# Optimization experiments

Measured on AMD Instinct MI355X. Metric: run time of the kernel, lower is better.

The kernel has to match this reference:

```python
import jax, jax.numpy as jnp
import numpy as np

B, I, K, O = 128, 64, 1024, 1024  # batch, kept in-axis, reduced in-axis, out-axis

def setup_inputs() -> dict:
    key = jax.random.key(0)
    k1, k2, k3 = jax.random.split(key, 3)
    stdv = 1.0 / np.sqrt(float(K))  # reduction covers in_shape[-1:] = [K]
    x = jax.random.normal(k1, (B, I, K), dtype=jnp.float32)
    weight = jax.random.uniform(k2, (O, I, K), dtype=jnp.float32, minval=-stdv, maxval=stdv)
    b = jax.random.uniform(k3, (O, I), dtype=jnp.float32, minval=-stdv, maxval=stdv)
    return {"x": x, "weight": weight, "b": b}

def reference(x, weight, b):
    # torch: unsqueeze x to [B,1,I,K], multiply by weight [O,I,K], sum last `reduction`=1
    # axes -> [B,O,I], add bias [O,I]. Expressed as a fused contraction:
    z = jnp.einsum('bik,oik->boi', x, weight)
    return z + b  # bias broadcasts over batch
```

## Files before the change

### kernel.cpp

```cpp
#include <hip/hip_runtime.h>

typedef __attribute__((ext_vector_type(8))) short  shortx8;
typedef __attribute__((ext_vector_type(4))) short  shortx4;
typedef __attribute__((ext_vector_type(4))) float  floatx4;

#define I_SZ 64
#define K_SZ 1024
#define IK   65536
#define OI   65536
#define BK   128
#define NKT  (K_SZ / BK)
#define LROW 256

__device__ __forceinline__ unsigned short f2bf(float f) {
    unsigned int u = __builtin_bit_cast(unsigned int, f);
    u += 0x7fffu + ((u >> 16) & 1u);
    return (unsigned short)(u >> 16);
}

__device__ __forceinline__ shortx4 cvt4(float4 a) {
    shortx4 r;
    r[0] = (short)f2bf(a.x); r[1] = (short)f2bf(a.y);
    r[2] = (short)f2bf(a.z); r[3] = (short)f2bf(a.w);
    return r;
}

__global__ __launch_bounds__(256, 2) void factlin_mfma2(
    const float* __restrict__ x, const float* __restrict__ w,
    const float* __restrict__ bias, float* __restrict__ out)
{
    __shared__ __align__(16) char lA[128 * LROW];
    __shared__ __align__(16) char lB[128 * LROW];

    const int wg   = blockIdx.x;
    const int nt   = wg & 7;
    const int i    = wg >> 3;
    const int tid  = threadIdx.x;
    const int lane = tid & 63;
    const int wid  = tid >> 6;
    const int wm   = wid >> 1;
    const int wn   = wid & 1;
    const int lrow = lane & 15;
    const int g    = lane >> 4;

    const float* gA = x + i * K_SZ;
    const float* gB = w + (nt * 128) * IK + i * K_SZ;

    floatx4 acc[4][4] = {};

    #pragma unroll 1
    for (int kt = 0; kt < NKT; ++kt) {
        __syncthreads();

        float4 buf[8];
        #pragma unroll
        for (int grp = 0; grp < 2; ++grp) {
            #pragma unroll
            for (int e = 0; e < 8; ++e) {
                const int c = (grp * 8 + e) * 256 + tid;
                buf[e] = *(const float4*)(gA + (c >> 5) * IK + kt * BK + (c & 31) * 4);
            }
            #pragma unroll
            for (int e = 0; e < 8; ++e) {
                const int c = (grp * 8 + e) * 256 + tid;
                const int row = c >> 5;
                const int off = row * LROW + (((c & 31) * 8) ^ ((row & 7) << 4));
                *(shortx4*)(lA + off) = cvt4(buf[e]);
            }
        }
        #pragma unroll
        for (int grp = 0; grp < 2; ++grp) {
            #pragma unroll
            for (int e = 0; e < 8; ++e) {
                const int c = (grp * 8 + e) * 256 + tid;
                buf[e] = *(const float4*)(gB + (c >> 5) * IK + kt * BK + (c & 31) * 4);
            }
            #pragma unroll
            for (int e = 0; e < 8; ++e) {
                const int c = (grp * 8 + e) * 256 + tid;
                const int row = c >> 5;
                const int off = row * LROW + (((c & 31) * 8) ^ ((row & 7) << 4));
                *(shortx4*)(lB + off) = cvt4(buf[e]);
            }
        }

        __syncthreads();

        #pragma unroll
        for (int ks = 0; ks < 4; ++ks) {
            shortx8 af[4], bf[4];
            #pragma unroll
            for (int mi = 0; mi < 4; ++mi) {
                const int row = wm * 64 + mi * 16 + lrow;
                const int off = row * LROW + ((ks * 64 + g * 16) ^ ((row & 7) << 4));
                af[mi] = *(const shortx8*)(lA + off);
            }
            #pragma unroll
            for (int ni = 0; ni < 4; ++ni) {
                const int row = wn * 64 + ni * 16 + lrow;
                const int off = row * LROW + ((ks * 64 + g * 16) ^ ((row & 7) << 4));
                bf[ni] = *(const shortx8*)(lB + off);
            }
            #pragma unroll
            for (int mi = 0; mi < 4; ++mi)
                #pragma unroll
                for (int ni = 0; ni < 4; ++ni)
                    acc[mi][ni] = __builtin_amdgcn_mfma_f32_16x16x32_bf16(
                        af[mi], bf[ni], acc[mi][ni], 0, 0, 0);
        }
    }

    const int obase = nt * 128 + wn * 64;
    float bv[4];
    #pragma unroll
    for (int ni = 0; ni < 4; ++ni)
        bv[ni] = bias[(obase + ni * 16 + lrow) * I_SZ + i];

    const int rb = wm * 64 + g * 4;
    #pragma unroll
    for (int mi = 0; mi < 4; ++mi) {
        #pragma unroll
        for (int ni = 0; ni < 4; ++ni) {
            const int ocol = obase + ni * 16 + lrow;
            float* op = out + (rb + mi * 16) * OI + ocol * I_SZ + i;
            #pragma unroll
            for (int r = 0; r < 4; ++r)
                op[r * OI] = acc[mi][ni][r] + bv[ni];
        }
    }
}

extern "C" void kernel_launch(void* const* d_in, const int* in_sizes, int n_in,
                              void* d_out, int out_size, void* d_ws, size_t ws_size,
                              hipStream_t stream) {
    const float* x  = (const float*)d_in[0];
    const float* w  = (const float*)d_in[1];
    const float* b  = (const float*)d_in[2];
    float* out      = (float*)d_out;

    factlin_mfma2<<<dim3(512), dim3(256), 0, stream>>>(x, w, b, out);
}
```

Before: 523.5 us.

## Double-buffer LDS tiles and prefetch next K tile into registers during MFMA

New measurement: 429.1 us. 18.0% less time.

```diff
diff --git a/kernel.cpp b/kernel.cpp
--- a/kernel.cpp
+++ b/kernel.cpp
@@ -8,9 +8,9 @@
 #define K_SZ 1024
 #define IK   65536
 #define OI   65536
-#define BK   128
+#define BK   64
 #define NKT  (K_SZ / BK)
-#define LROW 256
+#define LROW 128
 
 __device__ __forceinline__ unsigned short f2bf(float f) {
     unsigned int u = __builtin_bit_cast(unsigned int, f);
@@ -25,12 +25,12 @@
     return r;
 }
 
-__global__ __launch_bounds__(256, 2) void factlin_mfma2(
+__global__ __launch_bounds__(256, 2) void factlin_v3(
     const float* __restrict__ x, const float* __restrict__ w,
     const float* __restrict__ bias, float* __restrict__ out)
 {
-    __shared__ __align__(16) char lA[128 * LROW];
-    __shared__ __align__(16) char lB[128 * LROW];
+    __shared__ __align__(16) char lA[2][128 * LROW];
+    __shared__ __align__(16) char lB[2][128 * LROW];
 
     const int wg   = blockIdx.x;
     const int nt   = wg & 7;
@@ -46,60 +46,57 @@
     const float* gA = x + i * K_SZ;
     const float* gB = w + (nt * 128) * IK + i * K_SZ;
 
+    float4 vA[8], vB[8];
+
+    auto issue = [&](int kt) {
+        #pragma unroll
+        for (int e = 0; e < 8; ++e) {
+            const int c = e * 256 + tid;
+            vA[e] = *(const float4*)(gA + (c >> 4) * IK + kt * BK + (c & 15) * 4);
+        }
+        #pragma unroll
+        for (int e = 0; e < 8; ++e) {
+            const int c = e * 256 + tid;
+            vB[e] = *(const float4*)(gB + (c >> 4) * IK + kt * BK + (c & 15) * 4);
+        }
+    };
+    auto commit = [&](int buf) {
+        #pragma unroll
+        for (int e = 0; e < 8; ++e) {
+            const int c   = e * 256 + tid;
+            const int row = c >> 4;
+            const int off = row * LROW + (((c & 15) * 8) ^ ((row & 7) << 4));
+            *(shortx4*)(lA[buf] + off) = cvt4(vA[e]);
+            *(shortx4*)(lB[buf] + off) = cvt4(vB[e]);
+        }
+    };
+
+    issue(0);
+    commit(0);
+    __syncthreads();
+
     floatx4 acc[4][4] = {};
 
     #pragma unroll 1
     for (int kt = 0; kt < NKT; ++kt) {
-        __syncthreads();
+        const int cur = kt & 1;
 
-        float4 buf[8];
-        #pragma unroll
-        for (int grp = 0; grp < 2; ++grp) {
-            #pragma unroll
-            for (int e = 0; e < 8; ++e) {
-                const int c = (grp * 8 + e) * 256 + tid;
-                buf[e] = *(const float4*)(gA + (c >> 5) * IK + kt * BK + (c & 31) * 4);
-            }
-            #pragma unroll
-            for (int e = 0; e < 8; ++e) {
-                const int c = (grp * 8 + e) * 256 + tid;
-                const int row = c >> 5;
-                const int off = row * LROW + (((c & 31) * 8) ^ ((row & 7) << 4));
-                *(shortx4*)(lA + off) = cvt4(buf[e]);
-            }
-        }
-        #pragma unroll
-        for (int grp = 0; grp < 2; ++grp) {
-            #pragma unroll
-            for (int e = 0; e < 8; ++e) {
-                const int c = (grp * 8 + e) * 256 + tid;
-                buf[e] = *(const float4*)(gB + (c >> 5) * IK + kt * BK + (c & 31) * 4);
-            }
-            #pragma unroll
-            for (int e = 0; e < 8; ++e) {
-                const int c = (grp * 8 + e) * 256 + tid;
-                const int row = c >> 5;
-                const int off = row * LROW + (((c & 31) * 8) ^ ((row & 7) << 4));
-                *(shortx4*)(lB + off) = cvt4(buf[e]);
-            }
-        }
-
-        __syncthreads();
+        if (kt + 1 < NKT) issue(kt + 1);
 
         #pragma unroll
-        for (int ks = 0; ks < 4; ++ks) {
+        for (int ks = 0; ks < 2; ++ks) {
             shortx8 af[4], bf[4];
             #pragma unroll
             for (int mi = 0; mi < 4; ++mi) {
                 const int row = wm * 64 + mi * 16 + lrow;
                 const int off = row * LROW + ((ks * 64 + g * 16) ^ ((row & 7) << 4));
-                af[mi] = *(const shortx8*)(lA + off);
+                af[mi] = *(const shortx8*)(lA[cur] + off);
             }
             #pragma unroll
             for (int ni = 0; ni < 4; ++ni) {
                 const int row = wn * 64 + ni * 16 + lrow;
                 const int off = row * LROW + ((ks * 64 + g * 16) ^ ((row & 7) << 4));
-                bf[ni] = *(const shortx8*)(lB + off);
+                bf[ni] = *(const shortx8*)(lB[cur] + off);
             }
             #pragma unroll
             for (int mi = 0; mi < 4; ++mi)
@@ -108,6 +105,9 @@
                     acc[mi][ni] = __builtin_amdgcn_mfma_f32_16x16x32_bf16(
                         af[mi], bf[ni], acc[mi][ni], 0, 0, 0);
         }
+
+        if (kt + 1 < NKT) commit(cur ^ 1);
+        __syncthreads();
     }
 
     const int obase = nt * 128 + wn * 64;
@@ -138,5 +138,5 @@
     const float* b  = (const float*)d_in[2];
     float* out      = (float*)d_out;
 
-    factlin_mfma2<<<dim3(512), dim3(256), 0, stream>>>(x, w, b, out);
+    factlin_v3<<<dim3(512), dim3(256), 0, stream>>>(x, w, b, out);
 }
```
